# Optimization experiments

Hardware: AMD Instinct MI355X
Metric: run time of the kernel (lower is better)

Reference implementation:

```python
import jax, jax.numpy as jnp
import numpy as np

EPS = 1e-8  # torch CosineSimilarity default eps


def setup_inputs() -> dict:
    key = jax.random.key(0)
    ks = jax.random.split(key, 7)
    B, C, W, E, D = 64, 256, 256, 2048, 2048
    return {
        "x_img_dense": jax.random.normal(ks[0], (B, C, E), dtype=jnp.float32),
        "x_txt_dense": jax.random.normal(ks[1], (B, W, E), dtype=jnp.float32),
        "y_what_card_leader_choose": jax.random.normal(ks[2], (B, C), dtype=jnp.float32),
        "W_img1": jax.random.normal(ks[3], (D, E), dtype=jnp.float32) * 0.02,
        "b_img1": jax.random.normal(ks[4], (D,), dtype=jnp.float32) * 0.02,
        "W_words1": jax.random.normal(ks[5], (D, E), dtype=jnp.float32) * 0.02,
        "b_words1": jax.random.normal(ks[6], (D,), dtype=jnp.float32) * 0.02,
    }


def reference(x_img_dense, x_txt_dense, y_what_card_leader_choose,
              W_img1, b_img1, W_words1, b_words1):
    # Default path: img_layer=True, words_layer=True, comb_layer=False,
    # same_img_words_layer=False, gumbel=False, inference=False.
    xi = jnp.einsum('bce,de->bcd', x_img_dense, W_img1) + b_img1   # [B, C, D]
    xt = jnp.einsum('bwe,de->bwd', x_txt_dense, W_words1) + b_words1  # [B, W, D]

    # gather leader card embedding per batch element
    idx = jnp.argmax(y_what_card_leader_choose, axis=1)            # [B]
    leader = jnp.take_along_axis(xi, idx[:, None, None], axis=1)[:, 0, :]  # [B, D]

    # cosine similarity (dim=2 in torch): leader broadcast over words axis
    dot = jnp.einsum('bd,bwd->bw', leader, xt)                     # [B, W]
    denom = jnp.linalg.norm(leader, axis=-1, keepdims=True) * jnp.linalg.norm(xt, axis=-1)
    logits = dot / jnp.maximum(denom, EPS)                         # [B, W]

    # module returns softmax of `logits` (logits_final is dead code)
    return jax.nn.softmax(logits, axis=1)
```

## Files before the change

### kernel.cpp

```cpp
#include <hip/hip_runtime.h>
#include <hip/hip_bf16.h>
#include <stdint.h>

typedef unsigned short u16;
typedef __bf16 bf16x8 __attribute__((ext_vector_type(8)));
typedef float  f32x4  __attribute__((ext_vector_type(4)));
typedef float  fvec4  __attribute__((ext_vector_type(4)));

constexpr int NB = 64;
constexpr int NC = 256;
constexpr int NW = 256;
constexpr int NE = 2048;
constexpr int ND = 2048;
constexpr int MROWS = NB * NW;

constexpr int BM = 128, BN = 128, BK = 64;
constexpr int KSPLIT = 4;
constexpr int KSLICE = NE / KSPLIT;

constexpr int BM2 = 256, BN2 = 256;
constexpr int NT_K = NE / BK;
constexpr int NSLOT2 = ND / BN2;
constexpr int NSLOT1 = ND / BN;

constexpr size_t OFF_IDX  = 0;
constexpr size_t OFF_PART = 256;
constexpr size_t OFF_DOTP = 2097408;
constexpr size_t OFF_SSQP = 3145984;
constexpr size_t OFF_WW   = 4194560;
constexpr size_t OFF_XT   = 12583168;
constexpr size_t NEED_FULL = OFF_XT + 67108864ull;

__device__ __forceinline__ u16 f2bf(float f) {
    uint32_t u = __float_as_uint(f);
    u += 0x7fffu + ((u >> 16) & 1u);
    return (u16)(u >> 16);
}

__global__ void k_conv_argmax(const float* __restrict__ a, u16* __restrict__ da, int n4a,
                              const float* __restrict__ b, u16* __restrict__ db, int n4b,
                              const float* __restrict__ y, int* __restrict__ idx) {
    if (blockIdx.x == 0) {
        int t = threadIdx.x;
        int row = t >> 2, c = t & 3;
        float best = -3.4e38f; int bi = 0;
        for (int k = 0; k < 64; ++k) {
            int j = c + k * 4;
            float v = y[row * NC + j];
            if (v > best) { best = v; bi = j; }
        }
        #pragma unroll
        for (int off = 1; off <= 2; off <<= 1) {
            float ov = __shfl_xor(best, off, 64);
            int   oi = __shfl_xor(bi,   off, 64);
            if (ov > best || (ov == best && oi < bi)) { best = ov; bi = oi; }
        }
        if (c == 0) idx[row] = bi;
        return;
    }
    int i0 = (blockIdx.x - 1) * blockDim.x + threadIdx.x;
    int stride = (gridDim.x - 1) * blockDim.x;
    int n4 = n4a + n4b;
    for (int i = i0; i < n4; i += stride) {
        const fvec4* sp; ushort4* dp; int j;
        if (i < n4a) { sp = (const fvec4*)a; dp = (ushort4*)da; j = i; }
        else         { sp = (const fvec4*)b; dp = (ushort4*)db; j = i - n4a; }
        fvec4 v = __builtin_nontemporal_load(&sp[j]);
        ushort4 o = { f2bf(v.x), f2bf(v.y), f2bf(v.z), f2bf(v.w) };
        dp[j] = o;
    }
}

__global__ __launch_bounds__(256) void k_gemm0(
    const float* __restrict__ ximg, const int* __restrict__ idx,
    const float* __restrict__ Wimg, float* __restrict__ part)
{
    __shared__ __align__(16) u16 sA[BM * BK];
    __shared__ __align__(16) u16 sB[BN * BK];
    __shared__ int s_idx[64];

    const int t  = threadIdx.x;
    const int l  = t & 63;
    const int wv = t >> 6;
    const int wm = wv >> 1, wn = wv & 1;

    const int nt = blockIdx.x >> 2, ks = blockIdx.x & 3;
    const int n0 = nt * BN;
    const int kbase = ks * KSLICE;

    if (t < 64) s_idx[t] = idx[t];

    f32x4 acc[4][4];
    #pragma unroll
    for (int i = 0; i < 4; ++i)
        #pragma unroll
        for (int j = 0; j < 4; ++j) acc[i][j] = (f32x4){0.f, 0.f, 0.f, 0.f};

    const int lr = l >> 3, lp = l & 7;

    for (int k0 = kbase; k0 < kbase + KSLICE; k0 += BK) {
        __syncthreads();
        #pragma unroll
        for (int i = 0; i < 4; ++i) {
            int r = wv * 32 + i * 8 + lr;
            int g = lp ^ (r & 7);
            if (r < 64) {
                const float* src = ximg + ((size_t)r * NC + s_idx[r]) * NE + k0 + g * 8;
                float4 v0 = *(const float4*)src;
                float4 v1 = *(const float4*)(src + 4);
                uint4 ov;
                ov.x = (uint32_t)f2bf(v0.x) | ((uint32_t)f2bf(v0.y) << 16);
                ov.y = (uint32_t)f2bf(v0.z) | ((uint32_t)f2bf(v0.w) << 16);
                ov.z = (uint32_t)f2bf(v1.x) | ((uint32_t)f2bf(v1.y) << 16);
                ov.w = (uint32_t)f2bf(v1.z) | ((uint32_t)f2bf(v1.w) << 16);
                *(uint4*)&sA[r * BK + lp * 8] = ov;
            } else {
                *(uint4*)&sA[r * BK + lp * 8] = (uint4){0, 0, 0, 0};
            }
        }
        #pragma unroll
        for (int i = 0; i < 4; ++i) {
            int r = wv * 32 + i * 8 + lr;
            int g = lp ^ (r & 7);
            const float* src = Wimg + (size_t)(n0 + r) * NE + k0 + g * 8;
            float4 v0 = *(const float4*)src;
            float4 v1 = *(const float4*)(src + 4);
            uint4 ov;
            ov.x = (uint32_t)f2bf(v0.x) | ((uint32_t)f2bf(v0.y) << 16);
            ov.y = (uint32_t)f2bf(v0.z) | ((uint32_t)f2bf(v0.w) << 16);
            ov.z = (uint32_t)f2bf(v1.x) | ((uint32_t)f2bf(v1.y) << 16);
            ov.w = (uint32_t)f2bf(v1.z) | ((uint32_t)f2bf(v1.w) << 16);
            *(uint4*)&sB[r * BK + lp * 8] = ov;
        }
        __syncthreads();

        #pragma unroll
        for (int kk = 0; kk < 2; ++kk) {
            bf16x8 af[4], bfr[4];
            #pragma unroll
            for (int mi = 0; mi < 4; ++mi) {
                int ra = wm * 64 + mi * 16 + (l & 15);
                int g  = kk * 4 + (l >> 4);
                int p  = g ^ (ra & 7);
                af[mi] = *(const bf16x8*)&sA[ra * BK + p * 8];
            }
            #pragma unroll
            for (int nj = 0; nj < 4; ++nj) {
                int rb = wn * 64 + nj * 16 + (l & 15);
                int g  = kk * 4 + (l >> 4);
                int p  = g ^ (rb & 7);
                bfr[nj] = *(const bf16x8*)&sB[rb * BK + p * 8];
            }
            #pragma unroll
            for (int mi = 0; mi < 4; ++mi)
                #pragma unroll
                for (int nj = 0; nj < 4; ++nj)
                    acc[mi][nj] = __builtin_amdgcn_mfma_f32_16x16x32_bf16(
                        af[mi], bfr[nj], acc[mi][nj], 0, 0, 0);
        }
    }

    if (wm == 0) {
        const int quad = l >> 4, lc = l & 15;
        #pragma unroll
        for (int mi = 0; mi < 4; ++mi)
            #pragma unroll
            for (int r = 0; r < 4; ++r) {
                int m = mi * 16 + quad * 4 + r;
                #pragma unroll
                for (int nj = 0; nj < 4; ++nj) {
                    int n = n0 + wn * 64 + nj * 16 + lc;
                    part[((size_t)ks * NB + m) * ND + n] = acc[mi][nj][r];
                }
            }
    }
}

#define GLD(sp, dp) __builtin_amdgcn_global_load_lds( \
    (const __attribute__((address_space(1))) void*)(sp), \
    (__attribute__((address_space(3))) void*)(dp), 16, 0, 0)

#define STAGE_HALF(srcbase, h, kt, dstarr) do { \
    const u16* _s = (srcbase) + (size_t)(h) * 128 * NE + (size_t)(kt) * BK; \
    u16* _d = &(dstarr)[(h) * 8192 + dst0]; \
    GLD(_s, _d); \
    GLD(_s + (size_t)64 * NE, _d + 4096); \
} while (0)

#define RD_A(dst, mibase, pk) \
    _Pragma("unroll") for (int q = 0; q < 4; ++q) \
        dst[q] = *(const bf16x8*)&slA[arow + ((mibase) + q) * 1024 + (pk)];

#define RD_B(dst, pk) \
    _Pragma("unroll") for (int q = 0; q < 4; ++q) \
        dst[q] = *(const bf16x8*)&slB[brow + q * 1024 + (pk)];

#define MM(accbase, afr, bfr) \
    _Pragma("unroll") for (int q = 0; q < 4; ++q) \
        _Pragma("unroll") for (int nj = 0; nj < 4; ++nj) \
            acc[(accbase) + q][nj] = __builtin_amdgcn_mfma_f32_16x16x32_bf16( \
                afr[q], bfr[nj], acc[(accbase) + q][nj], 0, 0, 0);

#define TILE(S, tt) do { \
    const u16* slA = &lds[S][0][0]; \
    const u16* slB = &lds[S][1][0]; \
    bf16x8 af[4], bfr[4]; \
     \
    RD_A(af, 0, pk0); RD_B(bfr, pk0); \
    if ((tt) + 1 < NT_K) { \
        STAGE_HALF(Asrc, 0, (tt) + 1, lds[(S) ^ 1][0]); \
        STAGE_HALF(Asrc, 1, (tt) + 1, lds[(S) ^ 1][0]); \
    } \
    __builtin_amdgcn_s_setprio(1); MM(0, af, bfr); __builtin_amdgcn_s_setprio(0); \
     \
    RD_A(af, 4, pk0); \
    if ((tt) + 1 < NT_K) { \
        STAGE_HALF(Bsrc, 0, (tt) + 1, lds[(S) ^ 1][1]); \
        STAGE_HALF(Bsrc, 1, (tt) + 1, lds[(S) ^ 1][1]); \
    } \
    __builtin_amdgcn_s_setprio(1); MM(4, af, bfr); __builtin_amdgcn_s_setprio(0); \
     \
    RD_A(af, 0, pk1); RD_B(bfr, pk1); \
    __builtin_amdgcn_s_setprio(1); MM(0, af, bfr); __builtin_amdgcn_s_setprio(0); \
     \
    RD_A(af, 4, pk1); \
    __builtin_amdgcn_s_setprio(1); MM(4, af, bfr); __builtin_amdgcn_s_setprio(0); \
    __syncthreads();    \
} while (0)

__global__ __launch_bounds__(512, 2) void k_gemm1_8ph(
    const u16* __restrict__ A, const u16* __restrict__ B,
    const float* __restrict__ bwrd, const float* __restrict__ bimg,
    const float* __restrict__ part,
    float* __restrict__ dotp, float* __restrict__ ssqp)
{
    __shared__ __align__(16) u16 lds[2][2][16384];

    const int t  = threadIdx.x;
    const int l  = t & 63;
    const int wv = t >> 6;
    const int wm = wv >> 2;
    const int wn = wv & 3;

    const int mt = blockIdx.x >> 3;
    const int nt = blockIdx.x & 7;
    const int m0 = mt * BM2, n0 = nt * BN2;

    const int r0 = t >> 3;
    const int ge = ((t & 7) ^ (r0 & 7)) * 8;
    const u16* Asrc = A + (size_t)(m0 + r0) * NE + ge;
    const u16* Bsrc = B + (size_t)(n0 + r0) * NE + ge;
    const int dst0 = wv * 512;

    const int lc16 = l & 15, khi = l >> 4, lx = l & 7;
    const int pk0 = (khi ^ lx) * 8;
    const int pk1 = ((4 + khi) ^ lx) * 8;
    const int arow = (wm * 128 + lc16) * 64;
    const int brow = (wn * 64 + lc16) * 64;

    f32x4 acc[8][4];
    #pragma unroll
    for (int i = 0; i < 8; ++i)
        #pragma unroll
        for (int j = 0; j < 4; ++j) acc[i][j] = (f32x4){0.f, 0.f, 0.f, 0.f};

    STAGE_HALF(Asrc, 0, 0, lds[0][0]);
    STAGE_HALF(Asrc, 1, 0, lds[0][0]);
    STAGE_HALF(Bsrc, 0, 0, lds[0][1]);
    STAGE_HALF(Bsrc, 1, 0, lds[0][1]);
    __syncthreads();

    #pragma unroll 1
    for (int it = 0; it < NT_K / 2; ++it) {
        TILE(0, it * 2);
        TILE(1, it * 2 + 1);
    }

    const int quad = l >> 4, lc = l & 15;
    float bia[4], ldr[4];
    #pragma unroll
    for (int nj = 0; nj < 4; ++nj) {
        int n = n0 + wn * 64 + nj * 16 + lc;
        bia[nj] = bwrd[n];
        float ld = bimg[n];
        #pragma unroll
        for (int ks = 0; ks < KSPLIT; ++ks)
            ld += part[((size_t)ks * NB + mt) * ND + n];
        ldr[nj] = ld;
    }
    __syncthreads();
    float* sRed = (float*)&lds[0][0][0];
    #pragma unroll
    for (int mi = 0; mi < 8; ++mi) {
        #pragma unroll
        for (int r = 0; r < 4; ++r) {
            float pd = 0.f, ps = 0.f;
            #pragma unroll
            for (int nj = 0; nj < 4; ++nj) {
                float v = acc[mi][nj][r] + bia[nj];
                pd += ldr[nj] * v;
                ps += v * v;
            }
            #pragma unroll
            for (int off = 1; off <= 8; off <<= 1) {
                pd += __shfl_xor(pd, off, 64);
                ps += __shfl_xor(ps, off, 64);
            }
            if (lc == 0) {
                int row = mi * 16 + quad * 4 + r;
                sRed[(wm * 128 + row) * 4 + wn]        = pd;
                sRed[1024 + (wm * 128 + row) * 4 + wn] = ps;
            }
        }
    }
    __syncthreads();
    if (t < 256) {
        int m = m0 + t;
        const fvec4* s4 = (const fvec4*)sRed;
        fvec4 vd = s4[t], vs = s4[256 + t];
        dotp[(size_t)nt * MROWS + m] = vd.x + vd.y + vd.z + vd.w;
        ssqp[(size_t)nt * MROWS + m] = vs.x + vs.y + vs.z + vs.w;
    }
}

#undef TILE
#undef MM
#undef RD_B
#undef RD_A
#undef STAGE_HALF
#undef GLD

__global__ __launch_bounds__(256) void k_gemm1_f32(
    const float* __restrict__ Av, const float* __restrict__ Bv,
    const float* __restrict__ bwrd, const float* __restrict__ bimg,
    const float* __restrict__ part,
    float* __restrict__ dotp, float* __restrict__ ssqp)
{
    __shared__ __align__(16) u16 sA[BM * BK];
    __shared__ __align__(16) u16 sB[BN * BK];

    const int t  = threadIdx.x;
    const int l  = t & 63;
    const int wv = t >> 6;
    const int wm = wv >> 1, wn = wv & 1;

    const int mt = blockIdx.x >> 4;
    const int nt = blockIdx.x & 15;
    const int m0 = mt * BM, n0 = nt * BN;

    f32x4 acc[4][4];
    #pragma unroll
    for (int i = 0; i < 4; ++i)
        #pragma unroll
        for (int jj = 0; jj < 4; ++jj) acc[i][jj] = (f32x4){0.f, 0.f, 0.f, 0.f};

    const int lr = l >> 3, lp = l & 7;

    for (int k0 = 0; k0 < NE; k0 += BK) {
        __syncthreads();
        #pragma unroll
        for (int i = 0; i < 4; ++i) {
            int r = wv * 32 + i * 8 + lr;
            int g = lp ^ (r & 7);
            const float* src = Av + (size_t)(m0 + r) * NE + k0 + g * 8;
            float4 v0 = *(const float4*)src;
            float4 v1 = *(const float4*)(src + 4);
            uint4 ov;
            ov.x = (uint32_t)f2bf(v0.x) | ((uint32_t)f2bf(v0.y) << 16);
            ov.y = (uint32_t)f2bf(v0.z) | ((uint32_t)f2bf(v0.w) << 16);
            ov.z = (uint32_t)f2bf(v1.x) | ((uint32_t)f2bf(v1.y) << 16);
            ov.w = (uint32_t)f2bf(v1.z) | ((uint32_t)f2bf(v1.w) << 16);
            *(uint4*)&sA[r * BK + lp * 8] = ov;
        }
        #pragma unroll
        for (int i = 0; i < 4; ++i) {
            int r = wv * 32 + i * 8 + lr;
            int g = lp ^ (r & 7);
            const float* src = Bv + (size_t)(n0 + r) * NE + k0 + g * 8;
            float4 v0 = *(const float4*)src;
            float4 v1 = *(const float4*)(src + 4);
            uint4 ov;
            ov.x = (uint32_t)f2bf(v0.x) | ((uint32_t)f2bf(v0.y) << 16);
            ov.y = (uint32_t)f2bf(v0.z) | ((uint32_t)f2bf(v0.w) << 16);
            ov.z = (uint32_t)f2bf(v1.x) | ((uint32_t)f2bf(v1.y) << 16);
            ov.w = (uint32_t)f2bf(v1.z) | ((uint32_t)f2bf(v1.w) << 16);
            *(uint4*)&sB[r * BK + lp * 8] = ov;
        }
        __syncthreads();

        #pragma unroll
        for (int kk = 0; kk < 2; ++kk) {
            bf16x8 af[4], bfr[4];
            #pragma unroll
            for (int mi = 0; mi < 4; ++mi) {
                int ra = wm * 64 + mi * 16 + (l & 15);
                int g  = kk * 4 + (l >> 4);
                int p  = g ^ (ra & 7);
                af[mi] = *(const bf16x8*)&sA[ra * BK + p * 8];
            }
            #pragma unroll
            for (int nj = 0; nj < 4; ++nj) {
                int rb = wn * 64 + nj * 16 + (l & 15);
                int g  = kk * 4 + (l >> 4);
                int p  = g ^ (rb & 7);
                bfr[nj] = *(const bf16x8*)&sB[rb * BK + p * 8];
            }
            #pragma unroll
            for (int mi = 0; mi < 4; ++mi)
                #pragma unroll
                for (int nj = 0; nj < 4; ++nj)
                    acc[mi][nj] = __builtin_amdgcn_mfma_f32_16x16x32_bf16(
                        af[mi], bfr[nj], acc[mi][nj], 0, 0, 0);
        }
    }

    const int quad = l >> 4, lc = l & 15;
    const int bidx = m0 >> 8;
    float bia[4], ldr[4];
    #pragma unroll
    for (int nj = 0; nj < 4; ++nj) {
        int n = n0 + wn * 64 + nj * 16 + lc;
        bia[nj] = bwrd[n];
        float ld = bimg[n];
        #pragma unroll
        for (int ks = 0; ks < KSPLIT; ++ks)
            ld += part[((size_t)ks * NB + bidx) * ND + n];
        ldr[nj] = ld;
    }
    __syncthreads();
    float* sRed = (float*)sA;
    #pragma unroll
    for (int mi = 0; mi < 4; ++mi) {
        #pragma unroll
        for (int r = 0; r < 4; ++r) {
            float pd = 0.f, ps = 0.f;
            #pragma unroll
            for (int nj = 0; nj < 4; ++nj) {
                float v = acc[mi][nj][r] + bia[nj];
                pd += ldr[nj] * v;
                ps += v * v;
            }
            #pragma unroll
            for (int off = 1; off <= 8; off <<= 1) {
                pd += __shfl_xor(pd, off, 64);
                ps += __shfl_xor(ps, off, 64);
            }
            if (lc == 0) {
                int lm = mi * 16 + quad * 4 + r;
                sRed[(wm * 2 + wn) * 64 + lm]       = pd;
                sRed[256 + (wm * 2 + wn) * 64 + lm] = ps;
            }
        }
    }
    __syncthreads();
    if (t < 128) {
        int wmm = t >> 6, lm = t & 63;
        int m = m0 + wmm * 64 + lm;
        dotp[(size_t)nt * MROWS + m] =
            sRed[(wmm * 2 + 0) * 64 + lm] + sRed[(wmm * 2 + 1) * 64 + lm];
        ssqp[(size_t)nt * MROWS + m] =
            sRed[256 + (wmm * 2 + 0) * 64 + lm] + sRed[256 + (wmm * 2 + 1) * 64 + lm];
    }
}

__global__ void k_final(const float* __restrict__ part, const float* __restrict__ bimg,
                        const float* __restrict__ dotp, const float* __restrict__ ssqp,
                        float* __restrict__ out, int nslot) {
    int b = blockIdx.x, t = threadIdx.x;
    __shared__ float rsum[4], redm[4], reds[4];
    float s2 = 0.f;
    #pragma unroll
    for (int i = 0; i < 8; ++i) {
        int d = i * 256 + t;
        float ld = bimg[d];
        #pragma unroll
        for (int ks = 0; ks < KSPLIT; ++ks)
            ld += part[((size_t)ks * NB + b) * ND + d];
        s2 += ld * ld;
    }
    for (int off = 1; off < 64; off <<= 1) s2 += __shfl_xor(s2, off, 64);
    if ((t & 63) == 0) rsum[t >> 6] = s2;
    __syncthreads();
    float ln2 = rsum[0] + rsum[1] + rsum[2] + rsum[3];

    int m = b * NW + t;
    float dt = 0.f, sq = 0.f;
    for (int s = 0; s < nslot; ++s) {
        dt += dotp[(size_t)s * MROWS + m];
        sq += ssqp[(size_t)s * MROWS + m];
    }
    float dn = sqrtf(ln2) * sqrtf(sq);
    float lg = dt / fmaxf(dn, 1e-8f);
    float mx = lg;
    for (int off = 1; off < 64; off <<= 1) mx = fmaxf(mx, __shfl_xor(mx, off, 64));
    int wvi = t >> 6;
    if ((t & 63) == 0) redm[wvi] = mx;
    __syncthreads();
    mx = fmaxf(fmaxf(redm[0], redm[1]), fmaxf(redm[2], redm[3]));
    float e = __expf(lg - mx);
    float s = e;
    for (int off = 1; off < 64; off <<= 1) s += __shfl_xor(s, off, 64);
    if ((t & 63) == 0) reds[wvi] = s;
    __syncthreads();
    s = reds[0] + reds[1] + reds[2] + reds[3];
    out[m] = e / s;
}

extern "C" void kernel_launch(void* const* d_in, const int* in_sizes, int n_in,
                              void* d_out, int out_size, void* d_ws, size_t ws_size,
                              hipStream_t stream) {
    const float* ximg = (const float*)d_in[0];
    const float* xtxt = (const float*)d_in[1];
    const float* y    = (const float*)d_in[2];
    const float* Wimg = (const float*)d_in[3];
    const float* bimg = (const float*)d_in[4];
    const float* Wwrd = (const float*)d_in[5];
    const float* bwrd = (const float*)d_in[6];
    float* out = (float*)d_out;

    char* ws = (char*)d_ws;
    int*   idx  = (int*)(ws + OFF_IDX);
    float* part = (float*)(ws + OFF_PART);
    float* dotp = (float*)(ws + OFF_DOTP);
    float* ssqp = (float*)(ws + OFF_SSQP);
    u16*   WWb  = (u16*)(ws + OFF_WW);
    u16*   XTb  = (u16*)(ws + OFF_XT);

    const bool preconv = ws_size >= NEED_FULL;

    if (preconv) {
        k_conv_argmax<<<4097, 256, 0, stream>>>(Wwrd, WWb, ND * NE / 4,
                                                xtxt, XTb, MROWS * NE / 4, y, idx);
        k_gemm0<<<(ND / BN) * KSPLIT, 256, 0, stream>>>(ximg, idx, Wimg, part);
        k_gemm1_8ph<<<(MROWS / BM2) * (ND / BN2), 512, 0, stream>>>(
            XTb, WWb, bwrd, bimg, part, dotp, ssqp);
        k_final<<<NB, 256, 0, stream>>>(part, bimg, dotp, ssqp, out, NSLOT2);
    } else {
        k_conv_argmax<<<1, 256, 0, stream>>>(nullptr, nullptr, 0,
                                             nullptr, nullptr, 0, y, idx);
        k_gemm0<<<(ND / BN) * KSPLIT, 256, 0, stream>>>(ximg, idx, Wimg, part);
        k_gemm1_f32<<<(MROWS / BM) * (ND / BN), 256, 0, stream>>>(
            xtxt, Wwrd, bwrd, bimg, part, dotp, ssqp);
        k_final<<<NB, 256, 0, stream>>>(part, bimg, dotp, ssqp, out, NSLOT1);
    }
}
```

Baseline: 408.9 us.

## Fuse fp32-to-bf16 conversion of text activations into the main GEMM loader

The standalone pre-pass that converted the 128 MB fp32 text tensor to bf16 is removed. The main GEMM now loads fp32 A tiles into registers, converts them to bf16, and writes them to LDS itself, while B (the weights) is still pre-converted and staged with direct global-to-LDS loads. This avoids a full write-and-reread of a 64 MB bf16 copy. In exchange each tile reads twice as many bytes of A from global memory (fp32 rather than bf16, about 8x re-read across the 8 N-tiles), and the loads now go through registers, which costs VGPRs and adds conversion work inside the MFMA loop.

```diff
diff --git a/kernel.cpp b/kernel.cpp
--- a/kernel.cpp
+++ b/kernel.cpp
@@ -28,8 +28,7 @@
 constexpr size_t OFF_DOTP = 2097408;
 constexpr size_t OFF_SSQP = 3145984;
 constexpr size_t OFF_WW   = 4194560;
-constexpr size_t OFF_XT   = 12583168;
-constexpr size_t NEED_FULL = OFF_XT + 67108864ull;
+constexpr size_t NEED_MAIN = OFF_WW + (size_t)ND * NE * 2;
 
 __device__ __forceinline__ u16 f2bf(float f) {
     uint32_t u = __float_as_uint(f);
@@ -38,7 +37,6 @@
 }
 
 __global__ void k_conv_argmax(const float* __restrict__ a, u16* __restrict__ da, int n4a,
-                              const float* __restrict__ b, u16* __restrict__ db, int n4b,
                               const float* __restrict__ y, int* __restrict__ idx) {
     if (blockIdx.x == 0) {
         int t = threadIdx.x;
@@ -60,14 +58,10 @@
     }
     int i0 = (blockIdx.x - 1) * blockDim.x + threadIdx.x;
     int stride = (gridDim.x - 1) * blockDim.x;
-    int n4 = n4a + n4b;
-    for (int i = i0; i < n4; i += stride) {
-        const fvec4* sp; ushort4* dp; int j;
-        if (i < n4a) { sp = (const fvec4*)a; dp = (ushort4*)da; j = i; }
-        else         { sp = (const fvec4*)b; dp = (ushort4*)db; j = i - n4a; }
-        fvec4 v = __builtin_nontemporal_load(&sp[j]);
+    for (int i = i0; i < n4a; i += stride) {
+        fvec4 v = __builtin_nontemporal_load(&((const fvec4*)a)[i]);
         ushort4 o = { f2bf(v.x), f2bf(v.y), f2bf(v.z), f2bf(v.w) };
-        dp[j] = o;
+        ((ushort4*)da)[i] = o;
     }
 }
 
@@ -180,12 +174,29 @@
     (const __attribute__((address_space(1))) void*)(sp), \
     (__attribute__((address_space(3))) void*)(dp), 16, 0, 0)
 
-#define STAGE_HALF(srcbase, h, kt, dstarr) do { \
-    const u16* _s = (srcbase) + (size_t)(h) * 128 * NE + (size_t)(kt) * BK; \
+#define STAGE_B_HALF(h, kt, dstarr) do { \
+    const u16* _s = Bsrc + (size_t)(h) * 128 * NE + (size_t)(kt) * BK; \
     u16* _d = &(dstarr)[(h) * 8192 + dst0]; \
     GLD(_s, _d); \
     GLD(_s + (size_t)64 * NE, _d + 4096); \
 } while (0)
+
+#define ISSUE_A(kt) do { if ((kt) < NT_K) { \
+    _Pragma("unroll") for (int p = 0; p < 4; ++p) { \
+        const float* _s = Asrc + (size_t)((p >> 1) * 128 + (p & 1) * 64) * NE + (size_t)(kt) * BK; \
+        av0[p] = *(const float4*)_s; \
+        av1[p] = *(const float4*)(_s + 4); \
+    } } } while (0)
+
+#define WRITE_A(S2, kt) do { if ((kt) < NT_K) { \
+    _Pragma("unroll") for (int p = 0; p < 4; ++p) { \
+        bf16x8 w; \
+        w[0] = (__bf16)av0[p].x; w[1] = (__bf16)av0[p].y; \
+        w[2] = (__bf16)av0[p].z; w[3] = (__bf16)av0[p].w; \
+        w[4] = (__bf16)av1[p].x; w[5] = (__bf16)av1[p].y; \
+        w[6] = (__bf16)av1[p].z; w[7] = (__bf16)av1[p].w; \
+        *(bf16x8*)&lds[S2][0][(p >> 1) * 8192 + (p & 1) * 4096 + t * 8] = w; \
+    } } } while (0)
 
 #define RD_A(dst, mibase, pk) \
     _Pragma("unroll") for (int q = 0; q < 4; ++q) \
@@ -205,20 +216,19 @@
     const u16* slA = &lds[S][0][0]; \
     const u16* slB = &lds[S][1][0]; \
     bf16x8 af[4], bfr[4]; \
+    float4 av0[4], av1[4]; \
      \
     RD_A(af, 0, pk0); RD_B(bfr, pk0); \
+    ISSUE_A((tt) + 1); \
     if ((tt) + 1 < NT_K) { \
-        STAGE_HALF(Asrc, 0, (tt) + 1, lds[(S) ^ 1][0]); \
-        STAGE_HALF(Asrc, 1, (tt) + 1, lds[(S) ^ 1][0]); \
+        STAGE_B_HALF(0, (tt) + 1, lds[(S) ^ 1][1]); \
+        STAGE_B_HALF(1, (tt) + 1, lds[(S) ^ 1][1]); \
     } \
     __builtin_amdgcn_s_setprio(1); MM(0, af, bfr); __builtin_amdgcn_s_setprio(0); \
      \
     RD_A(af, 4, pk0); \
-    if ((tt) + 1 < NT_K) { \
-        STAGE_HALF(Bsrc, 0, (tt) + 1, lds[(S) ^ 1][1]); \
-        STAGE_HALF(Bsrc, 1, (tt) + 1, lds[(S) ^ 1][1]); \
-    } \
     __builtin_amdgcn_s_setprio(1); MM(4, af, bfr); __builtin_amdgcn_s_setprio(0); \
+    WRITE_A((S) ^ 1, (tt) + 1); \
      \
     RD_A(af, 0, pk1); RD_B(bfr, pk1); \
     __builtin_amdgcn_s_setprio(1); MM(0, af, bfr); __builtin_amdgcn_s_setprio(0); \
@@ -229,7 +239,7 @@
 } while (0)
 
 __global__ __launch_bounds__(512, 2) void k_gemm1_8ph(
-    const u16* __restrict__ A, const u16* __restrict__ B,
+    const float* __restrict__ A, const u16* __restrict__ B,
     const float* __restrict__ bwrd, const float* __restrict__ bimg,
     const float* __restrict__ part,
     float* __restrict__ dotp, float* __restrict__ ssqp)
@@ -248,8 +258,8 @@
 
     const int r0 = t >> 3;
     const int ge = ((t & 7) ^ (r0 & 7)) * 8;
-    const u16* Asrc = A + (size_t)(m0 + r0) * NE + ge;
-    const u16* Bsrc = B + (size_t)(n0 + r0) * NE + ge;
+    const float* Asrc = A + (size_t)(m0 + r0) * NE + ge;
+    const u16*   Bsrc = B + (size_t)(n0 + r0) * NE + ge;
     const int dst0 = wv * 512;
 
     const int lc16 = l & 15, khi = l >> 4, lx = l & 7;
@@ -264,10 +274,13 @@
         #pragma unroll
         for (int j = 0; j < 4; ++j) acc[i][j] = (f32x4){0.f, 0.f, 0.f, 0.f};
 
-    STAGE_HALF(Asrc, 0, 0, lds[0][0]);
-    STAGE_HALF(Asrc, 1, 0, lds[0][0]);
-    STAGE_HALF(Bsrc, 0, 0, lds[0][1]);
-    STAGE_HALF(Bsrc, 1, 0, lds[0][1]);
+    {
+        float4 av0[4], av1[4];
+        ISSUE_A(0);
+        STAGE_B_HALF(0, 0, lds[0][1]);
+        STAGE_B_HALF(1, 0, lds[0][1]);
+        WRITE_A(0, 0);
+    }
     __syncthreads();
 
     #pragma unroll 1
@@ -327,7 +340,9 @@
 #undef MM
 #undef RD_B
 #undef RD_A
-#undef STAGE_HALF
+#undef WRITE_A
+#undef ISSUE_A
+#undef STAGE_B_HALF
 #undef GLD
 
 __global__ __launch_bounds__(256) void k_gemm1_f32(
@@ -524,20 +539,17 @@
     float* dotp = (float*)(ws + OFF_DOTP);
     float* ssqp = (float*)(ws + OFF_SSQP);
     u16*   WWb  = (u16*)(ws + OFF_WW);
-    u16*   XTb  = (u16*)(ws + OFF_XT);
-
-    const bool preconv = ws_size >= NEED_FULL;
-
-    if (preconv) {
-        k_conv_argmax<<<4097, 256, 0, stream>>>(Wwrd, WWb, ND * NE / 4,
-                                                xtxt, XTb, MROWS * NE / 4, y, idx);
+
+    const bool main_path = ws_size >= NEED_MAIN;
+
+    if (main_path) {
+        k_conv_argmax<<<2049, 256, 0, stream>>>(Wwrd, WWb, ND * NE / 4, y, idx);
         k_gemm0<<<(ND / BN) * KSPLIT, 256, 0, stream>>>(ximg, idx, Wimg, part);
         k_gemm1_8ph<<<(MROWS / BM2) * (ND / BN2), 512, 0, stream>>>(
-            XTb, WWb, bwrd, bimg, part, dotp, ssqp);
+            xtxt, WWb, bwrd, bimg, part, dotp, ssqp);
         k_final<<<NB, 256, 0, stream>>>(part, bimg, dotp, ssqp, out, NSLOT2);
     } else {
-        k_conv_argmax<<<1, 256, 0, stream>>>(nullptr, nullptr, 0,
-                                             nullptr, nullptr, 0, y, idx);
+        k_conv_argmax<<<1, 256, 0, stream>>>(nullptr, nullptr, 0, y, idx);
         k_gemm0<<<(ND / BN) * KSPLIT, 256, 0, stream>>>(ximg, idx, Wimg, part);
         k_gemm1_f32<<<(MROWS / BM) * (ND / BN), 256, 0, stream>>>(
             xtxt, Wwrd, bwrd, bimg, part, dotp, ssqp);
```

Result: slower. 641.3 us (+56.8%).

## Fuse argmax, leader GEMM and bf16 conversion into one front kernel; swizzle GEMM blocks

Applied to the files above, without the earlier changes.

Merges the argmax, the leader-row GEMM (gemm0) and the fp32-to-bf16 conversion of the text activations and word weights into a single kernel. The first 64 blocks each compute the argmax redundantly into shared memory and then run the gemm0 tile, while the remaining 2048 blocks run a grid-stride conversion loop. This removes one launch and the idx round trip through global memory, and lets gemm0 overlap with the conversion. It also remaps block indices in the main bf16 GEMM so that consecutive blocks share the same N tile, which is meant to improve L2 reuse of the weight tiles. The cost is that every gemm0 block now repeats the argmax work, and the conversion grid is halved.

```diff
diff --git a/kernel.cpp b/kernel.cpp
--- a/kernel.cpp
+++ b/kernel.cpp
@@ -22,6 +22,9 @@
 constexpr int NT_K = NE / BK;
 constexpr int NSLOT2 = ND / BN2;
 constexpr int NSLOT1 = ND / BN;
+
+constexpr int G0_BLOCKS = 64;
+constexpr int CONV_BLOCKS = 2048;
 
 constexpr size_t OFF_IDX  = 0;
 constexpr size_t OFF_PART = 256;
@@ -37,11 +40,41 @@
     return (u16)(u >> 16);
 }
 
-__global__ void k_conv_argmax(const float* __restrict__ a, u16* __restrict__ da, int n4a,
-                              const float* __restrict__ b, u16* __restrict__ db, int n4b,
-                              const float* __restrict__ y, int* __restrict__ idx) {
-    if (blockIdx.x == 0) {
-        int t = threadIdx.x;
+__global__ __launch_bounds__(256) void k_front(
+    const float* __restrict__ ximg, const float* __restrict__ Wimg,
+    const float* __restrict__ y, float* __restrict__ part,
+    const float* __restrict__ xtxt, u16* __restrict__ XTb, int n4x,
+    const float* __restrict__ Wwrd, u16* __restrict__ WWb, int n4w)
+{
+    if (blockIdx.x >= G0_BLOCKS) {
+        int i0 = (int)(blockIdx.x - G0_BLOCKS) * 256 + threadIdx.x;
+        int stride = (int)(gridDim.x - G0_BLOCKS) * 256;
+        int n4 = n4x + n4w;
+        for (int i = i0; i < n4; i += stride) {
+            const fvec4* sp; ushort4* dp; int j;
+            if (i < n4x) { sp = (const fvec4*)xtxt; dp = (ushort4*)XTb; j = i; }
+            else         { sp = (const fvec4*)Wwrd; dp = (ushort4*)WWb; j = i - n4x; }
+            fvec4 v = __builtin_nontemporal_load(&sp[j]);
+            ushort4 o = { f2bf(v.x), f2bf(v.y), f2bf(v.z), f2bf(v.w) };
+            dp[j] = o;
+        }
+        return;
+    }
+
+    __shared__ __align__(16) u16 sA[BM * BK];
+    __shared__ __align__(16) u16 sB[BN * BK];
+    __shared__ int s_idx[64];
+
+    const int t  = threadIdx.x;
+    const int l  = t & 63;
+    const int wv = t >> 6;
+    const int wm = wv >> 1, wn = wv & 1;
+
+    const int nt = blockIdx.x >> 2, ks = blockIdx.x & 3;
+    const int n0 = nt * BN;
+    const int kbase = ks * KSLICE;
+
+    {
         int row = t >> 2, c = t & 3;
         float best = -3.4e38f; int bi = 0;
         for (int k = 0; k < 64; ++k) {
@@ -55,40 +88,8 @@
             int   oi = __shfl_xor(bi,   off, 64);
             if (ov > best || (ov == best && oi < bi)) { best = ov; bi = oi; }
         }
-        if (c == 0) idx[row] = bi;
-        return;
-    }
-    int i0 = (blockIdx.x - 1) * blockDim.x + threadIdx.x;
-    int stride = (gridDim.x - 1) * blockDim.x;
-    int n4 = n4a + n4b;
-    for (int i = i0; i < n4; i += stride) {
-        const fvec4* sp; ushort4* dp; int j;
-        if (i < n4a) { sp = (const fvec4*)a; dp = (ushort4*)da; j = i; }
-        else         { sp = (const fvec4*)b; dp = (ushort4*)db; j = i - n4a; }
-        fvec4 v = __builtin_nontemporal_load(&sp[j]);
-        ushort4 o = { f2bf(v.x), f2bf(v.y), f2bf(v.z), f2bf(v.w) };
-        dp[j] = o;
-    }
-}
-
-__global__ __launch_bounds__(256) void k_gemm0(
-    const float* __restrict__ ximg, const int* __restrict__ idx,
-    const float* __restrict__ Wimg, float* __restrict__ part)
-{
-    __shared__ __align__(16) u16 sA[BM * BK];
-    __shared__ __align__(16) u16 sB[BN * BK];
-    __shared__ int s_idx[64];
-
-    const int t  = threadIdx.x;
-    const int l  = t & 63;
-    const int wv = t >> 6;
-    const int wm = wv >> 1, wn = wv & 1;
-
-    const int nt = blockIdx.x >> 2, ks = blockIdx.x & 3;
-    const int n0 = nt * BN;
-    const int kbase = ks * KSLICE;
-
-    if (t < 64) s_idx[t] = idx[t];
+        if (c == 0) s_idx[row] = bi;
+    }
 
     f32x4 acc[4][4];
     #pragma unroll
@@ -242,8 +243,10 @@
     const int wm = wv >> 2;
     const int wn = wv & 3;
 
-    const int mt = blockIdx.x >> 3;
-    const int nt = blockIdx.x & 7;
+    const int bid = blockIdx.x;
+    const int swz = (bid & 7) * 64 + (bid >> 3);
+    const int mt = swz >> 3;
+    const int nt = swz & 7;
     const int m0 = mt * BM2, n0 = nt * BN2;
 
     const int r0 = t >> 3;
@@ -519,7 +522,6 @@
     float* out = (float*)d_out;
 
     char* ws = (char*)d_ws;
-    int*   idx  = (int*)(ws + OFF_IDX);
     float* part = (float*)(ws + OFF_PART);
     float* dotp = (float*)(ws + OFF_DOTP);
     float* ssqp = (float*)(ws + OFF_SSQP);
@@ -529,16 +531,18 @@
     const bool preconv = ws_size >= NEED_FULL;
 
     if (preconv) {
-        k_conv_argmax<<<4097, 256, 0, stream>>>(Wwrd, WWb, ND * NE / 4,
-                                                xtxt, XTb, MROWS * NE / 4, y, idx);
-        k_gemm0<<<(ND / BN) * KSPLIT, 256, 0, stream>>>(ximg, idx, Wimg, part);
+        k_front<<<G0_BLOCKS + CONV_BLOCKS, 256, 0, stream>>>(
+            ximg, Wimg, y, part,
+            xtxt, XTb, MROWS * NE / 4,
+            Wwrd, WWb, ND * NE / 4);
         k_gemm1_8ph<<<(MROWS / BM2) * (ND / BN2), 512, 0, stream>>>(
             XTb, WWb, bwrd, bimg, part, dotp, ssqp);
         k_final<<<NB, 256, 0, stream>>>(part, bimg, dotp, ssqp, out, NSLOT2);
     } else {
-        k_conv_argmax<<<1, 256, 0, stream>>>(nullptr, nullptr, 0,
-                                             nullptr, nullptr, 0, y, idx);
-        k_gemm0<<<(ND / BN) * KSPLIT, 256, 0, stream>>>(ximg, idx, Wimg, part);
+        k_front<<<G0_BLOCKS, 256, 0, stream>>>(
+            ximg, Wimg, y, part,
+            nullptr, nullptr, 0,
+            nullptr, nullptr, 0);
         k_gemm1_f32<<<(MROWS / BM) * (ND / BN), 256, 0, stream>>>(
             xtxt, Wwrd, bwrd, bimg, part, dotp, ssqp);
         k_final<<<NB, 256, 0, stream>>>(part, bimg, dotp, ssqp, out, NSLOT1);
```

After: 381.3 us. 6.8% less time.
